# Performance work log

Hardware: AMD Instinct MI355X
Metric: run time of the kernel (lower is better)

The kernel has to match this reference:

```python
import jax, jax.numpy as jnp
import numpy as np
from jax import lax

B, C, IC, H, W = 4, 64, 32, 64, 64


def _conv(x, w, b, stride, pad):
    y = lax.conv_general_dilated(
        x, w, (stride, stride), [(pad, pad), (pad, pad)],
        dimension_numbers=('NCHW', 'OIHW', 'NCHW'))
    return y + b[None, :, None, None]


def setup_inputs() -> dict:
    key = jax.random.key(0)
    ks = jax.random.split(key, 15)
    s = 0.05
    inp = {
        'x': jax.random.normal(ks[0], (B, C, H, W), jnp.float32),
        # GEunit convs (3x3)
        'd1_w': jax.random.normal(ks[1], (C, C, 3, 3), jnp.float32) * s,
        'd1_b': jax.random.normal(ks[2], (C,), jnp.float32) * s,
        'd2_w': jax.random.normal(ks[3], (C, C, 3, 3), jnp.float32) * s,
        'd2_b': jax.random.normal(ks[4], (C,), jnp.float32) * s,
        'd3_w': jax.random.normal(ks[5], (C, C, 3, 3), jnp.float32) * s,
        'd3_b': jax.random.normal(ks[6], (C,), jnp.float32) * s,
        # 1x1 projections
        'g_w': jax.random.normal(ks[7], (IC, C, 1, 1), jnp.float32) * s,
        'g_b': jax.random.normal(ks[8], (IC,), jnp.float32) * s,
        'th_w': jax.random.normal(ks[9], (IC, C, 1, 1), jnp.float32) * s,
        'th_b': jax.random.normal(ks[10], (IC,), jnp.float32) * s,
        'ph_w': jax.random.normal(ks[11], (IC, C, 1, 1), jnp.float32) * s,
        'ph_b': jax.random.normal(ks[12], (IC,), jnp.float32) * s,
        # output projection (zero-init in original; random here for nontrivial baseline)
        'w_w': jax.random.normal(ks[13], (C, IC, 1, 1), jnp.float32) * s,
        'w_b': jax.random.normal(ks[14], (C,), jnp.float32) * s,
    }
    return inp


def _forward(x, d1_w, d1_b, d2_w, d2_b, d3_w, d3_b,
             g_w, g_b, th_w, th_b, ph_w, ph_b, w_w, w_b):
    lrelu = lambda v: jnp.where(v >= 0, v, 0.2 * v)
    y = lrelu(_conv(x, d1_w, d1_b, 2, 1))
    y = lrelu(_conv(y, d2_w, d2_b, 2, 1))
    y = _conv(y, d3_w, d3_b, 2, 1)
    y = jax.image.resize(y, (x.shape[0], x.shape[1], x.shape[2], x.shape[3]),
                         method='bilinear')  # align_corners=False equivalent
    am = jax.nn.sigmoid(y) * x  # attention_map, [B,C,H,W]

    b, c, h, w = am.shape
    n = h * w
    g_x = _conv(am, g_w, g_b, 1, 0).reshape(b, IC, n)      # [B,IC,N]
    theta = _conv(am, th_w, th_b, 1, 0).reshape(b, IC, n)  # [B,IC,N]
    phi = _conv(am, ph_w, ph_b, 1, 0).reshape(b, IC, n)    # [B,IC,N]

    # f[b,i,j] = theta[:, i] . phi[:, j];  softmax over dim=1 (the i axis)
    f = jnp.einsum('bci,bcj->bij', theta, phi)             # [B,N,N]
    f_div_C = jax.nn.softmax(f, axis=1)
    y2 = jnp.einsum('bij,bjc->bic', f_div_C, g_x.transpose(0, 2, 1))  # [B,N,IC]
    y2 = y2.transpose(0, 2, 1).reshape(b, IC, h, w)

    W_y = _conv(y2, w_w, w_b, 1, 0)
    z = W_y + am
    return z * x


def reference(x, d1_w, d1_b, d2_w, d2_b, d3_w, d3_b,
              g_w, g_b, th_w, th_b, ph_w, ph_b, w_w, w_b):
    return _forward(x, d1_w, d1_b, d2_w, d2_b, d3_w, d3_b,
                    g_w, g_b, th_w, th_b, ph_w, ph_b, w_w, w_b)
```

## Files before the change

kernel.cpp:

```cpp
#include <hip/hip_runtime.h>

#define B_ 4
#define C_ 64
#define IC_ 32
#define N_ 4096
#define LOG2E 1.44269504088896341f

typedef __attribute__((ext_vector_type(8))) short short8;
typedef __attribute__((ext_vector_type(4))) float floatx4;

__device__ __forceinline__ unsigned short f2bf(float f) {
  unsigned u = __float_as_uint(f);
  u += 0x7FFFu + ((u >> 16) & 1u);
  return (unsigned short)(u >> 16);
}
__device__ __forceinline__ float bf2f(unsigned short h) {
  return __uint_as_float(((unsigned)h) << 16);
}

__global__ void __launch_bounds__(256) pack_xw_k(
    const float* __restrict__ x, unsigned short* __restrict__ xclp,
    const float* __restrict__ d1_w, const float* __restrict__ d2_w, const float* __restrict__ d3_w,
    const float* __restrict__ th_w, const float* __restrict__ ph_w, const float* __restrict__ g_w,
    const float* __restrict__ th_b, const float* __restrict__ ph_b, const float* __restrict__ g_b,
    unsigned short* __restrict__ wpk, unsigned short* __restrict__ wproj, float* __restrict__ bproj,
    unsigned short* __restrict__ y1clp, unsigned short* __restrict__ y2clp)
{
  __shared__ float s[64][65];
  const int t = threadIdx.x;
  if (blockIdx.x < 256) {
    const int b = blockIdx.x >> 6, h = blockIdx.x & 63;
    for (int idx = t; idx < 4096; idx += 256) {
      int c = idx >> 6, w = idx & 63;
      s[c][w] = x[((size_t)(b * 64 + c)) * 4096 + h * 64 + w];
    }
    __syncthreads();
    for (int idx = t; idx < 4096; idx += 256) {
      int w = idx >> 6, c = idx & 63;
      xclp[(((size_t)b * 66 + h + 1) * 66 + (w + 1)) * 64 + c] = f2bf(s[c][w]);
    }
  } else {
    const int tid = (blockIdx.x - 256) * 256 + t;
    for (int idx = tid; idx < 3 * 36864; idx += 16 * 256) {
      int cv = idx / 36864, r = idx % 36864;
      int tap = r / 4096, r2 = r % 4096;
      int oc = r2 >> 6, ic = r2 & 63;
      const float* src = (cv == 0) ? d1_w : (cv == 1) ? d2_w : d3_w;
      wpk[(size_t)cv * 36864 + tap * 4096 + oc * 64 + ic] = f2bf(src[oc * 576 + ic * 9 + tap]);
    }
    for (int idx = tid; idx < 6144; idx += 16 * 256) {
      int m = idx >> 6, ic = idx & 63;
      float v = (m < 32) ? LOG2E * th_w[m * 64 + ic]
              : (m < 64) ? ph_w[(m - 32) * 64 + ic]
                         : g_w[(m - 64) * 64 + ic];
      wproj[m * 64 + ic] = f2bf(v);
    }
    for (int m = tid; m < 96; m += 16 * 256) {
      bproj[m] = (m < 32) ? LOG2E * th_b[m] : (m < 64) ? ph_b[m - 32] : g_b[m - 64];
    }
    const uint4 z4 = {0u, 0u, 0u, 0u};
    for (int idx = tid; idx < 4 * 4356; idx += 4096) {
      int r = idx % 4356, h = r / 66, w = r % 66;
      if (h == 0 || h == 65 || w == 0 || w == 65) {
        uint4* d = reinterpret_cast<uint4*>(xclp + (size_t)idx * 64);
#pragma unroll
        for (int q = 0; q < 8; ++q) d[q] = z4;
      }
    }
    for (int idx = tid; idx < 4 * 1156; idx += 4096) {
      int r = idx % 1156, h = r / 34, w = r % 34;
      if (h == 0 || h == 33 || w == 0 || w == 33) {
        uint4* d = reinterpret_cast<uint4*>(y1clp + (size_t)idx * 64);
#pragma unroll
        for (int q = 0; q < 8; ++q) d[q] = z4;
      }
    }
    for (int idx = tid; idx < 4 * 324; idx += 4096) {
      int r = idx % 324, h = r / 18, w = r % 18;
      if (h == 0 || h == 17 || w == 0 || w == 17) {
        uint4* d = reinterpret_cast<uint4*>(y2clp + (size_t)idx * 64);
#pragma unroll
        for (int q = 0; q < 8; ++q) d[q] = z4;
      }
    }
  }
}

template<int IN_PW, int OUT_H, bool LRELU, bool OUT_BF16>
__global__ void __launch_bounds__(64) convmf_k(
    const unsigned short* __restrict__ xin, const unsigned short* __restrict__ wp,
    const float* __restrict__ bias, unsigned short* __restrict__ obf,
    float* __restrict__ of32)
{
  constexpr int NTILES = OUT_H * OUT_H / 16;
  const int lane = threadIdx.x;
  const int n15 = lane & 15, quad = lane >> 4;
  int bx = blockIdx.x;
  const int octile = bx & 3; bx >>= 2;
  const int otile = bx % NTILES;
  const int b = bx / NTILES;
  const int o = otile * 16 + n15;
  const int oh = o / OUT_H, ow = o % OUT_H;
  const unsigned short* xb = xin + (size_t)b * IN_PW * IN_PW * 64;
  floatx4 acc = {0.f, 0.f, 0.f, 0.f};
#pragma unroll
  for (int tap = 0; tap < 9; ++tap) {
    const int kh = tap / 3, kw = tap % 3;
    const unsigned short* xpix = xb + ((size_t)(oh * 2 + kh) * IN_PW + (ow * 2 + kw)) * 64;
#pragma unroll
    for (int ks = 0; ks < 2; ++ks) {
      short8 af = *reinterpret_cast<const short8*>(
          wp + ((size_t)tap * 64 + octile * 16 + n15) * 64 + ks * 32 + quad * 8);
      short8 bf = *reinterpret_cast<const short8*>(xpix + ks * 32 + quad * 8);
      acc = __builtin_amdgcn_mfma_f32_16x16x32_bf16(af, bf, acc, 0, 0, 0);
    }
  }
  const float4 bv = *reinterpret_cast<const float4*>(bias + octile * 16 + quad * 4);
  float v[4] = {acc[0] + bv.x, acc[1] + bv.y, acc[2] + bv.z, acc[3] + bv.w};
  if (LRELU) {
#pragma unroll
    for (int r = 0; r < 4; ++r) v[r] = (v[r] >= 0.f) ? v[r] : 0.2f * v[r];
  }
  if (OUT_BF16) {
    constexpr int OPW = OUT_H + 2;
    unsigned short pk[4];
#pragma unroll
    for (int r = 0; r < 4; ++r) pk[r] = f2bf(v[r]);
    *reinterpret_cast<uint2*>(
        obf + (((size_t)b * OPW + oh + 1) * OPW + (ow + 1)) * 64 + octile * 16 + quad * 4) =
        *reinterpret_cast<uint2*>(pk);
  } else {
    *reinterpret_cast<float4*>(
        of32 + ((size_t)b * OUT_H * OUT_H + o) * 64 + octile * 16 + quad * 4) =
        *reinterpret_cast<float4*>(v);
  }
}

__global__ void __launch_bounds__(256) upsproj_k(
    const unsigned short* __restrict__ y2clp, const unsigned short* __restrict__ wp3,
    const float* __restrict__ b3, const float* __restrict__ x,
    const unsigned short* __restrict__ wproj, const float* __restrict__ bproj,
    unsigned short* __restrict__ am_cl, unsigned short* __restrict__ thph,
    unsigned short* __restrict__ g16)
{
  const int b = blockIdx.x >> 6, oh = blockIdx.x & 63;
  const int t = threadIdx.x;
  __shared__ float s0[512], s1[512];
  __shared__ unsigned short s_am[64][72];
  float sh = (oh + 0.5f) * 0.125f - 0.5f;
  float fh = floorf(sh); float ah = sh - fh; int h0 = (int)fh;
  int h0c = min(7, max(0, h0)), h1c = min(7, max(0, h0 + 1));
  {
    const int wave = t >> 6, lane = t & 63;
    const int n15 = lane & 15, quad = lane >> 4;
    const int hrow = (n15 < 8) ? h0c : h1c;
    const int ow8 = n15 & 7;
    const unsigned short* xb2 = y2clp + (size_t)b * 18 * 18 * 64;
    floatx4 acc = {0.f, 0.f, 0.f, 0.f};
#pragma unroll
    for (int tap = 0; tap < 9; ++tap) {
      const int kh = tap / 3, kw = tap % 3;
      const unsigned short* xpix = xb2 + ((size_t)(hrow * 2 + kh) * 18 + (ow8 * 2 + kw)) * 64;
#pragma unroll
      for (int ks = 0; ks < 2; ++ks) {
        short8 af = *reinterpret_cast<const short8*>(
            wp3 + ((size_t)tap * 64 + wave * 16 + n15) * 64 + ks * 32 + quad * 8);
        short8 bf = *reinterpret_cast<const short8*>(xpix + ks * 32 + quad * 8);
        acc = __builtin_amdgcn_mfma_f32_16x16x32_bf16(af, bf, acc, 0, 0, 0);
      }
    }
    const float4 bv = *reinterpret_cast<const float4*>(b3 + wave * 16 + quad * 4);
    float4 st = {acc[0] + bv.x, acc[1] + bv.y, acc[2] + bv.z, acc[3] + bv.w};
    float* dst = (n15 < 8) ? s0 : s1;
    *reinterpret_cast<float4*>(&dst[(size_t)ow8 * 64 + wave * 16 + quad * 4]) = st;
  }
  __syncthreads();
  {
    const int ow = t >> 2, cq = t & 3;
    float sw = (ow + 0.5f) * 0.125f - 0.5f;
    float fw = floorf(sw); float aw = sw - fw; int w0 = (int)fw;
    int w0c = min(7, max(0, w0)), w1c = min(7, max(0, w0 + 1));
    const int n = oh * 64 + ow;
    const float* xb = x + (size_t)b * 64 * 4096 + n;
    unsigned short* ap = am_cl + ((size_t)b * N_ + n) * 64 + cq * 16;
#pragma unroll
    for (int u = 0; u < 4; ++u) {
      int c0 = cq * 16 + u * 4;
      float4 a00 = *reinterpret_cast<const float4*>(&s0[w0c * 64 + c0]);
      float4 a01 = *reinterpret_cast<const float4*>(&s0[w1c * 64 + c0]);
      float4 a10 = *reinterpret_cast<const float4*>(&s1[w0c * 64 + c0]);
      float4 a11 = *reinterpret_cast<const float4*>(&s1[w1c * 64 + c0]);
      float i0[4] = {a00.x * (1.f - aw) + a01.x * aw, a00.y * (1.f - aw) + a01.y * aw,
                     a00.z * (1.f - aw) + a01.z * aw, a00.w * (1.f - aw) + a01.w * aw};
      float i1[4] = {a10.x * (1.f - aw) + a11.x * aw, a10.y * (1.f - aw) + a11.y * aw,
                     a10.z * (1.f - aw) + a11.z * aw, a10.w * (1.f - aw) + a11.w * aw};
      unsigned short pk[4];
#pragma unroll
      for (int vi = 0; vi < 4; ++vi) {
        float vv = i0[vi] * (1.f - ah) + i1[vi] * ah;
        float xv = xb[(size_t)(c0 + vi) * 4096];
        float sig = 1.f / (1.f + __expf(-vv));
        pk[vi] = f2bf(sig * xv);
      }
      uint2 pkt = *reinterpret_cast<uint2*>(pk);
      *reinterpret_cast<uint2*>(ap + u * 4) = pkt;
      *reinterpret_cast<uint2*>(&s_am[ow][c0]) = pkt;
    }
  }
  __syncthreads();
  const int wave = t >> 6, lane = t & 63;
  const int n15 = lane & 15, quad = lane >> 4;
  const int n = oh * 64 + wave * 16 + n15;
  const unsigned short* srow = &s_am[wave * 16 + n15][0];
  const short8 bf0 = *reinterpret_cast<const short8*>(srow + quad * 8);
  const short8 bf1 = *reinterpret_cast<const short8*>(srow + 32 + quad * 8);
#pragma unroll
  for (int mt = 0; mt < 6; ++mt) {
    short8 a0 = *reinterpret_cast<const short8*>(wproj + ((size_t)mt * 16 + n15) * 64 + quad * 8);
    short8 a1 = *reinterpret_cast<const short8*>(wproj + ((size_t)mt * 16 + n15) * 64 + 32 + quad * 8);
    floatx4 acc = {0.f, 0.f, 0.f, 0.f};
    acc = __builtin_amdgcn_mfma_f32_16x16x32_bf16(a0, bf0, acc, 0, 0, 0);
    acc = __builtin_amdgcn_mfma_f32_16x16x32_bf16(a1, bf1, acc, 0, 0, 0);
    const float4 bv = *reinterpret_cast<const float4*>(bproj + mt * 16 + quad * 4);
    float v[4] = {acc[0] + bv.x, acc[1] + bv.y, acc[2] + bv.z, acc[3] + bv.w};
    if (mt < 4) {
      unsigned short pk[4];
#pragma unroll
      for (int r = 0; r < 4; ++r) pk[r] = f2bf(v[r]);
      *reinterpret_cast<uint2*>(thph + ((size_t)b * N_ + n) * 64 + mt * 16 + quad * 4) =
          *reinterpret_cast<uint2*>(pk);
    } else {
#pragma unroll
      for (int r = 0; r < 4; ++r)
        g16[((size_t)b * 32 + (mt - 4) * 16 + quad * 4 + r) * N_ + n] = f2bf(v[r]);
    }
  }
}

__global__ void __launch_bounds__(256) attn_stats_k(
    const unsigned short* __restrict__ thph, float* __restrict__ lpart)
{
  const int b  = blockIdx.y;
  const int iz = blockIdx.z;
  const int t = threadIdx.x, wave = t >> 6, lane = t & 63;
  const int n15 = lane & 15, quad = lane >> 4;
  const int jw = blockIdx.x * 512 + wave * 128;
  const unsigned short* base = thph + (size_t)b * N_ * 64;
  short8 bv[8];
#pragma unroll
  for (int v = 0; v < 8; ++v)
    bv[v] = *reinterpret_cast<const short8*>(base + (size_t)(jw + v * 16 + n15) * 64 + 32 + quad * 8);
  float ls[8];
#pragma unroll
  for (int v = 0; v < 8; ++v) ls[v] = 0.f;
  const unsigned short* ap = base + (size_t)(iz * 256 + n15) * 64 + quad * 8;
  short8 ac = *reinterpret_cast<const short8*>(ap);
  for (int st = 0; st < 16; ++st) {
    short8 an = *reinterpret_cast<const short8*>(ap + (size_t)((st < 15) ? st + 1 : st) * 1024);
#pragma unroll
    for (int v = 0; v < 8; ++v) {
      floatx4 z = {0.f, 0.f, 0.f, 0.f};
      z = __builtin_amdgcn_mfma_f32_16x16x32_bf16(ac, bv[v], z, 0, 0, 0);
      ls[v] += (__builtin_amdgcn_exp2f(z[0]) + __builtin_amdgcn_exp2f(z[1]))
             + (__builtin_amdgcn_exp2f(z[2]) + __builtin_amdgcn_exp2f(z[3]));
    }
    ac = an;
  }
#pragma unroll
  for (int v = 0; v < 8; ++v) {
    ls[v] += __shfl_xor(ls[v], 16);
    ls[v] += __shfl_xor(ls[v], 32);
  }
  if (quad == 0) {
#pragma unroll
    for (int v = 0; v < 8; ++v)
      lpart[((size_t)iz * B_ + b) * N_ + jw + v * 16 + n15] = ls[v];
  }
}

#define PHI_PITCH 40
#define G_PITCH   136
__global__ void __launch_bounds__(256, 2) attn_pv_k(
    const unsigned short* __restrict__ thph, const unsigned short* __restrict__ g16,
    const float* __restrict__ lpart, unsigned short* __restrict__ y2p)
{
  const int b  = blockIdx.y;
  const int jq = blockIdx.z;
  const int t = threadIdx.x, wave = t >> 6, lane = t & 63;
  const int n15 = lane & 15, quad = lane >> 4;
  const int iw = blockIdx.x * 128 + wave * 32;
  const unsigned short* base = thph + (size_t)b * N_ * 64;
  const unsigned short* gs   = g16  + (size_t)b * 32 * N_;
  __shared__ unsigned short phi_lds[2][128 * PHI_PITCH];
  __shared__ unsigned short g_lds[2][32 * G_PITCH];
  __shared__ float rl_lds[1024];

  const int jbase = jq * 1024;
  for (int jj = t; jj < 1024; jj += 256) {
    float l = 0.f;
#pragma unroll
    for (int iz = 0; iz < 16; ++iz) l += lpart[((size_t)iz * B_ + b) * N_ + jbase + jj];
    rl_lds[jj] = 1.f / l;
  }

  const short8 bth0 = *reinterpret_cast<const short8*>(base + (size_t)(iw + n15) * 64 + quad * 8);
  const short8 bth1 = *reinterpret_cast<const short8*>(base + (size_t)(iw + 16 + n15) * 64 + quad * 8);
  floatx4 Y00 = {0.f, 0.f, 0.f, 0.f}, Y01 = {0.f, 0.f, 0.f, 0.f};
  floatx4 Y10 = {0.f, 0.f, 0.f, 0.f}, Y11 = {0.f, 0.f, 0.f, 0.f};

  const int rphi = wave * 32 + (lane >> 2), cph = lane & 3;
  const int cg   = wave * 8  + (lane >> 4), chg = lane & 15;

  uint4 sp0, sp1, sg0, sg1;
  sp0 = *reinterpret_cast<const uint4*>(base + (size_t)(jbase + rphi) * 64 + 32 + cph * 8);
  sp1 = *reinterpret_cast<const uint4*>(base + (size_t)(jbase + rphi + 16) * 64 + 32 + cph * 8);
  sg0 = *reinterpret_cast<const uint4*>(gs + (size_t)cg * N_ + jbase + chg * 8);
  sg1 = *reinterpret_cast<const uint4*>(gs + (size_t)(cg + 4) * N_ + jbase + chg * 8);
  __syncthreads();

#define PV_WRITE_STAGE(BUF, CHN)                                                     \
  {                                                                                  \
    *reinterpret_cast<uint4*>(&phi_lds[BUF][rphi * PHI_PITCH + cph * 8]) = sp0;      \
    *reinterpret_cast<uint4*>(&phi_lds[BUF][(rphi + 16) * PHI_PITCH + cph * 8]) = sp1;\
    const int jloc = (CHN) * 128 + chg * 8;                                          \
    float4 r0 = *reinterpret_cast<const float4*>(&rl_lds[jloc]);                     \
    float4 r1 = *reinterpret_cast<const float4*>(&rl_lds[jloc + 4]);                 \
    union U8s { uint4 u4; unsigned short us[8]; } ua, ub, oa, ob_;                   \
    ua.u4 = sg0; ub.u4 = sg1;                                                        \
    oa.us[0] = f2bf(bf2f(ua.us[0]) * r0.x); oa.us[1] = f2bf(bf2f(ua.us[1]) * r0.y);  \
    oa.us[2] = f2bf(bf2f(ua.us[2]) * r0.z); oa.us[3] = f2bf(bf2f(ua.us[3]) * r0.w);  \
    oa.us[4] = f2bf(bf2f(ua.us[4]) * r1.x); oa.us[5] = f2bf(bf2f(ua.us[5]) * r1.y);  \
    oa.us[6] = f2bf(bf2f(ua.us[6]) * r1.z); oa.us[7] = f2bf(bf2f(ua.us[7]) * r1.w);  \
    ob_.us[0] = f2bf(bf2f(ub.us[0]) * r0.x); ob_.us[1] = f2bf(bf2f(ub.us[1]) * r0.y);\
    ob_.us[2] = f2bf(bf2f(ub.us[2]) * r0.z); ob_.us[3] = f2bf(bf2f(ub.us[3]) * r0.w);\
    ob_.us[4] = f2bf(bf2f(ub.us[4]) * r1.x); ob_.us[5] = f2bf(bf2f(ub.us[5]) * r1.y);\
    ob_.us[6] = f2bf(bf2f(ub.us[6]) * r1.z); ob_.us[7] = f2bf(bf2f(ub.us[7]) * r1.w);\
    *reinterpret_cast<uint4*>(&g_lds[BUF][cg * G_PITCH + chg * 8]) = oa.u4;          \
    *reinterpret_cast<uint4*>(&g_lds[BUF][(cg + 4) * G_PITCH + chg * 8]) = ob_.u4;   \
  }

  PV_WRITE_STAGE(0, 0)
  __syncthreads();

  int j0 = jbase;
  for (int ch = 0; ch < 8; ++ch, j0 += 128) {
    const int cur = ch & 1;
    if (ch < 7) {
      const int jn = j0 + 128;
      sp0 = *reinterpret_cast<const uint4*>(base + (size_t)(jn + rphi) * 64 + 32 + cph * 8);
      sp1 = *reinterpret_cast<const uint4*>(base + (size_t)(jn + rphi + 16) * 64 + 32 + cph * 8);
      sg0 = *reinterpret_cast<const uint4*>(gs + (size_t)cg * N_ + jn + chg * 8);
      sg1 = *reinterpret_cast<const uint4*>(gs + (size_t)(cg + 4) * N_ + jn + chg * 8);
    }
    const unsigned short* phb = &phi_lds[cur][0];
    const unsigned short* glb = &g_lds[cur][0];
#pragma unroll
    for (int sg = 0; sg < 4; ++sg) {
      unsigned pk0[4], pk1[4];
#pragma unroll
      for (int jtl = 0; jtl < 2; ++jtl) {
        const int jt = sg * 2 + jtl;
        short8 aph = *reinterpret_cast<const short8*>(phb + (jt * 16 + n15) * PHI_PITCH + quad * 8);
        floatx4 z0 = {0.f, 0.f, 0.f, 0.f}, z1 = {0.f, 0.f, 0.f, 0.f};
        z0 = __builtin_amdgcn_mfma_f32_16x16x32_bf16(aph, bth0, z0, 0, 0, 0);
        z1 = __builtin_amdgcn_mfma_f32_16x16x32_bf16(aph, bth1, z1, 0, 0, 0);
        float a0 = __builtin_amdgcn_exp2f(z0[0]), a1 = __builtin_amdgcn_exp2f(z0[1]);
        float a2 = __builtin_amdgcn_exp2f(z0[2]), a3 = __builtin_amdgcn_exp2f(z0[3]);
        float b0f = __builtin_amdgcn_exp2f(z1[0]), b1f = __builtin_amdgcn_exp2f(z1[1]);
        float b2f = __builtin_amdgcn_exp2f(z1[2]), b3f = __builtin_amdgcn_exp2f(z1[3]);
        pk0[jtl * 2 + 0] = __builtin_amdgcn_perm(__float_as_uint(a1), __float_as_uint(a0), 0x07060302);
        pk0[jtl * 2 + 1] = __builtin_amdgcn_perm(__float_as_uint(a3), __float_as_uint(a2), 0x07060302);
        pk1[jtl * 2 + 0] = __builtin_amdgcn_perm(__float_as_uint(b1f), __float_as_uint(b0f), 0x07060302);
        pk1[jtl * 2 + 1] = __builtin_amdgcn_perm(__float_as_uint(b3f), __float_as_uint(b2f), 0x07060302);
      }
      union { unsigned u[4]; short8 v; } pa0, pa1, gb0, gb1;
      pa0.u[0] = pk0[0]; pa0.u[1] = pk0[1]; pa0.u[2] = pk0[2]; pa0.u[3] = pk0[3];
      pa1.u[0] = pk1[0]; pa1.u[1] = pk1[1]; pa1.u[2] = pk1[2]; pa1.u[3] = pk1[3];
      const unsigned short* gr0 = glb + n15 * G_PITCH + sg * 32 + quad * 4;
      const unsigned short* gr1 = glb + (16 + n15) * G_PITCH + sg * 32 + quad * 4;
      uint2 lo0 = *reinterpret_cast<const uint2*>(gr0);
      uint2 hi0 = *reinterpret_cast<const uint2*>(gr0 + 16);
      uint2 lo1 = *reinterpret_cast<const uint2*>(gr1);
      uint2 hi1 = *reinterpret_cast<const uint2*>(gr1 + 16);
      gb0.u[0] = lo0.x; gb0.u[1] = lo0.y; gb0.u[2] = hi0.x; gb0.u[3] = hi0.y;
      gb1.u[0] = lo1.x; gb1.u[1] = lo1.y; gb1.u[2] = hi1.x; gb1.u[3] = hi1.y;
      Y00 = __builtin_amdgcn_mfma_f32_16x16x32_bf16(pa0.v, gb0.v, Y00, 0, 0, 0);
      Y01 = __builtin_amdgcn_mfma_f32_16x16x32_bf16(pa0.v, gb1.v, Y01, 0, 0, 0);
      Y10 = __builtin_amdgcn_mfma_f32_16x16x32_bf16(pa1.v, gb0.v, Y10, 0, 0, 0);
      Y11 = __builtin_amdgcn_mfma_f32_16x16x32_bf16(pa1.v, gb1.v, Y11, 0, 0, 0);
    }
    if (ch < 7) {
      const int nb = cur ^ 1;
      PV_WRITE_STAGE(nb, ch + 1)
    }
    __syncthreads();
  }
#undef PV_WRITE_STAGE
  unsigned w00[2], w01[2], w10[2], w11[2];
  w00[0] = ((unsigned)f2bf(Y00[1]) << 16) | f2bf(Y00[0]);
  w00[1] = ((unsigned)f2bf(Y00[3]) << 16) | f2bf(Y00[2]);
  w01[0] = ((unsigned)f2bf(Y01[1]) << 16) | f2bf(Y01[0]);
  w01[1] = ((unsigned)f2bf(Y01[3]) << 16) | f2bf(Y01[2]);
  w10[0] = ((unsigned)f2bf(Y10[1]) << 16) | f2bf(Y10[0]);
  w10[1] = ((unsigned)f2bf(Y10[3]) << 16) | f2bf(Y10[2]);
  w11[0] = ((unsigned)f2bf(Y11[1]) << 16) | f2bf(Y11[0]);
  w11[1] = ((unsigned)f2bf(Y11[3]) << 16) | f2bf(Y11[2]);
  const size_t orow = ((size_t)jq * B_ + b) * 32;
  *reinterpret_cast<uint2*>(y2p + (orow + n15) * N_ + iw + quad * 4) =
      *reinterpret_cast<uint2*>(w00);
  *reinterpret_cast<uint2*>(y2p + (orow + 16 + n15) * N_ + iw + quad * 4) =
      *reinterpret_cast<uint2*>(w01);
  *reinterpret_cast<uint2*>(y2p + (orow + n15) * N_ + iw + 16 + quad * 4) =
      *reinterpret_cast<uint2*>(w10);
  *reinterpret_cast<uint2*>(y2p + (orow + 16 + n15) * N_ + iw + 16 + quad * 4) =
      *reinterpret_cast<uint2*>(w11);
}

__global__ void __launch_bounds__(256) final_k(
    const unsigned short* __restrict__ y2p, const float* __restrict__ w_w,
    const float* __restrict__ w_b, const unsigned short* __restrict__ am_cl,
    const float* __restrict__ x, float* __restrict__ out)
{
  const int n0 = (blockIdx.x * 256 + threadIdx.x) * 2;
  const int o0 = blockIdx.y * 8;
  const int b  = blockIdx.z;
  float a0[8], a1[8];
#pragma unroll
  for (int u = 0; u < 8; ++u) { a0[u] = w_b[o0 + u]; a1[u] = a0[u]; }
  for (int c = 0; c < 32; ++c) {
    float s0 = 0.f, s1 = 0.f;
#pragma unroll
    for (int ph = 0; ph < 4; ++ph) {
      unsigned v = *reinterpret_cast<const unsigned*>(
          y2p + (((size_t)ph * B_ + b) * 32 + c) * N_ + n0);
      s0 += bf2f((unsigned short)(v & 0xffffu));
      s1 += bf2f((unsigned short)(v >> 16));
    }
#pragma unroll
    for (int u = 0; u < 8; ++u) {
      float wv = w_w[(o0 + u) * 32 + c];
      a0[u] += wv * s0; a1[u] += wv * s1;
    }
  }
  const short8 am0 = *reinterpret_cast<const short8*>(am_cl + ((size_t)b * N_ + n0) * 64 + o0);
  const short8 am1 = *reinterpret_cast<const short8*>(am_cl + ((size_t)b * N_ + n0 + 1) * 64 + o0);
#pragma unroll
  for (int u = 0; u < 8; ++u) {
    size_t off = ((size_t)b * 64 + o0 + u) * N_ + n0;
    float2 xv = *reinterpret_cast<const float2*>(x + off);
    float2 ov;
    ov.x = (a0[u] + bf2f((unsigned short)am0[u])) * xv.x;
    ov.y = (a1[u] + bf2f((unsigned short)am1[u])) * xv.y;
    *reinterpret_cast<float2*>(out + off) = ov;
  }
}

extern "C" void kernel_launch(void* const* d_in, const int* in_sizes, int n_in,
                              void* d_out, int out_size, void* d_ws, size_t ws_size,
                              hipStream_t stream) {
  const float* x    = (const float*)d_in[0];
  const float* d1_w = (const float*)d_in[1];
  const float* d1_b = (const float*)d_in[2];
  const float* d2_w = (const float*)d_in[3];
  const float* d2_b = (const float*)d_in[4];
  const float* d3_w = (const float*)d_in[5];
  const float* d3_b = (const float*)d_in[6];
  const float* g_w  = (const float*)d_in[7];
  const float* g_b  = (const float*)d_in[8];
  const float* th_w = (const float*)d_in[9];
  const float* th_b = (const float*)d_in[10];
  const float* ph_w = (const float*)d_in[11];
  const float* ph_b = (const float*)d_in[12];
  const float* w_w  = (const float*)d_in[13];
  const float* w_b  = (const float*)d_in[14];
  float* out = (float*)d_out;

  char* p = (char*)d_ws;
  unsigned short* am_cl = (unsigned short*)p;  p += (size_t)B_ * N_ * 64 * 2;
  unsigned short* thph  = (unsigned short*)p;  p += (size_t)B_ * N_ * 64 * 2;
  unsigned short* g16   = (unsigned short*)p;  p += (size_t)B_ * 32 * N_ * 2;
  float* lpart          = (float*)p;           p += (size_t)16 * B_ * N_ * 4;
  unsigned short* y2p   = (unsigned short*)p;  p += (size_t)4 * B_ * 32 * N_ * 2;
  unsigned short* wpk   = (unsigned short*)p;  p += (size_t)3 * 36864 * 2;
  unsigned short* wproj = (unsigned short*)p;  p += (size_t)96 * 64 * 2;
  float* bproj          = (float*)p;           p += (size_t)96 * 4;
  unsigned short* xclp  = (unsigned short*)p;  p += (size_t)B_ * 66 * 66 * 64 * 2;
  unsigned short* y1clp = (unsigned short*)p;  p += (size_t)B_ * 34 * 34 * 64 * 2;
  unsigned short* y2clp = (unsigned short*)p;  p += (size_t)B_ * 18 * 18 * 64 * 2;

  pack_xw_k<<<272, 256, 0, stream>>>(x, xclp, d1_w, d2_w, d3_w, th_w, ph_w, g_w,
                                     th_b, ph_b, g_b, wpk, wproj, bproj, y1clp, y2clp);
  convmf_k<66, 32, true,  true ><<<1024, 64, 0, stream>>>(xclp,  wpk,         d1_b, y1clp, nullptr);
  convmf_k<34, 16, true,  true ><<<256,  64, 0, stream>>>(y1clp, wpk + 36864, d2_b, y2clp, nullptr);
  upsproj_k<<<256, 256, 0, stream>>>(y2clp, wpk + 2 * 36864, d3_b, x, wproj, bproj,
                                     am_cl, thph, g16);
  attn_stats_k<<<dim3(8, 4, 16), 256, 0, stream>>>(thph, lpart);
  attn_pv_k<<<dim3(32, 4, 4), 256, 0, stream>>>(thph, g16, lpart, y2p);
  final_k<<<dim3(8, 8, 4), 256, 0, stream>>>(y2p, w_w, w_b, am_cl, x, out);
}
```

Measured before the change: 152.5 us.

## Retile conv, attention PV and final kernels; pad upsample LDS rows

The stride-2 conv kernel now computes two 16-channel output tiles per wave, reusing each input fragment across two MFMAs and halving the grid. The attention PV kernel gives each wave 64 query rows instead of 32 and splits the key axis into 8 partitions of 512 instead of 4 of 1024, so it issues more MFMAs per loaded phi/g tile and writes twice as many partial outputs. The final kernel first reduces the 8 partials into shared memory and then has each thread compute 16 output channels. The upsample LDS rows are padded from 64 to 68 floats to avoid bank conflicts. In exchange there are more registers per wave in the PV kernel and more partial-sum traffic.

```diff
diff --git a/kernel.cpp b/kernel.cpp
--- a/kernel.cpp
+++ b/kernel.cpp
@@ -86,54 +86,52 @@
   }
 }
 
-template<int IN_PW, int OUT_H, bool LRELU, bool OUT_BF16>
+template<int IN_PW, int OUT_H>
 __global__ void __launch_bounds__(64) convmf_k(
     const unsigned short* __restrict__ xin, const unsigned short* __restrict__ wp,
-    const float* __restrict__ bias, unsigned short* __restrict__ obf,
-    float* __restrict__ of32)
+    const float* __restrict__ bias, unsigned short* __restrict__ obf)
 {
   constexpr int NTILES = OUT_H * OUT_H / 16;
   const int lane = threadIdx.x;
   const int n15 = lane & 15, quad = lane >> 4;
   int bx = blockIdx.x;
-  const int octile = bx & 3; bx >>= 2;
+  const int opair = bx & 1; bx >>= 1;
   const int otile = bx % NTILES;
   const int b = bx / NTILES;
   const int o = otile * 16 + n15;
   const int oh = o / OUT_H, ow = o % OUT_H;
   const unsigned short* xb = xin + (size_t)b * IN_PW * IN_PW * 64;
-  floatx4 acc = {0.f, 0.f, 0.f, 0.f};
+  floatx4 acc0 = {0.f, 0.f, 0.f, 0.f}, acc1 = {0.f, 0.f, 0.f, 0.f};
 #pragma unroll
   for (int tap = 0; tap < 9; ++tap) {
     const int kh = tap / 3, kw = tap % 3;
     const unsigned short* xpix = xb + ((size_t)(oh * 2 + kh) * IN_PW + (ow * 2 + kw)) * 64;
 #pragma unroll
     for (int ks = 0; ks < 2; ++ks) {
-      short8 af = *reinterpret_cast<const short8*>(
-          wp + ((size_t)tap * 64 + octile * 16 + n15) * 64 + ks * 32 + quad * 8);
       short8 bf = *reinterpret_cast<const short8*>(xpix + ks * 32 + quad * 8);
-      acc = __builtin_amdgcn_mfma_f32_16x16x32_bf16(af, bf, acc, 0, 0, 0);
-    }
-  }
-  const float4 bv = *reinterpret_cast<const float4*>(bias + octile * 16 + quad * 4);
-  float v[4] = {acc[0] + bv.x, acc[1] + bv.y, acc[2] + bv.z, acc[3] + bv.w};
-  if (LRELU) {
-#pragma unroll
-    for (int r = 0; r < 4; ++r) v[r] = (v[r] >= 0.f) ? v[r] : 0.2f * v[r];
-  }
-  if (OUT_BF16) {
-    constexpr int OPW = OUT_H + 2;
-    unsigned short pk[4];
-#pragma unroll
-    for (int r = 0; r < 4; ++r) pk[r] = f2bf(v[r]);
-    *reinterpret_cast<uint2*>(
-        obf + (((size_t)b * OPW + oh + 1) * OPW + (ow + 1)) * 64 + octile * 16 + quad * 4) =
-        *reinterpret_cast<uint2*>(pk);
-  } else {
-    *reinterpret_cast<float4*>(
-        of32 + ((size_t)b * OUT_H * OUT_H + o) * 64 + octile * 16 + quad * 4) =
-        *reinterpret_cast<float4*>(v);
-  }
+      short8 af0 = *reinterpret_cast<const short8*>(
+          wp + ((size_t)tap * 64 + (opair * 2 + 0) * 16 + n15) * 64 + ks * 32 + quad * 8);
+      short8 af1 = *reinterpret_cast<const short8*>(
+          wp + ((size_t)tap * 64 + (opair * 2 + 1) * 16 + n15) * 64 + ks * 32 + quad * 8);
+      acc0 = __builtin_amdgcn_mfma_f32_16x16x32_bf16(af0, bf, acc0, 0, 0, 0);
+      acc1 = __builtin_amdgcn_mfma_f32_16x16x32_bf16(af1, bf, acc1, 0, 0, 0);
+    }
+  }
+  constexpr int OPW = OUT_H + 2;
+  const float4 bv0 = *reinterpret_cast<const float4*>(bias + (opair * 2 + 0) * 16 + quad * 4);
+  const float4 bv1 = *reinterpret_cast<const float4*>(bias + (opair * 2 + 1) * 16 + quad * 4);
+  float v0[4] = {acc0[0] + bv0.x, acc0[1] + bv0.y, acc0[2] + bv0.z, acc0[3] + bv0.w};
+  float v1[4] = {acc1[0] + bv1.x, acc1[1] + bv1.y, acc1[2] + bv1.z, acc1[3] + bv1.w};
+  unsigned short pk0[4], pk1[4];
+#pragma unroll
+  for (int r = 0; r < 4; ++r) {
+    v0[r] = (v0[r] >= 0.f) ? v0[r] : 0.2f * v0[r];
+    v1[r] = (v1[r] >= 0.f) ? v1[r] : 0.2f * v1[r];
+    pk0[r] = f2bf(v0[r]); pk1[r] = f2bf(v1[r]);
+  }
+  unsigned short* orow = obf + (((size_t)b * OPW + oh + 1) * OPW + (ow + 1)) * 64;
+  *reinterpret_cast<uint2*>(orow + (opair * 2 + 0) * 16 + quad * 4) = *reinterpret_cast<uint2*>(pk0);
+  *reinterpret_cast<uint2*>(orow + (opair * 2 + 1) * 16 + quad * 4) = *reinterpret_cast<uint2*>(pk1);
 }
 
 __global__ void __launch_bounds__(256) upsproj_k(
@@ -145,7 +143,7 @@
 {
   const int b = blockIdx.x >> 6, oh = blockIdx.x & 63;
   const int t = threadIdx.x;
-  __shared__ float s0[512], s1[512];
+  __shared__ float s0[8 * 68], s1[8 * 68];
   __shared__ unsigned short s_am[64][72];
   float sh = (oh + 0.5f) * 0.125f - 0.5f;
   float fh = floorf(sh); float ah = sh - fh; int h0 = (int)fh;
@@ -172,7 +170,7 @@
     const float4 bv = *reinterpret_cast<const float4*>(b3 + wave * 16 + quad * 4);
     float4 st = {acc[0] + bv.x, acc[1] + bv.y, acc[2] + bv.z, acc[3] + bv.w};
     float* dst = (n15 < 8) ? s0 : s1;
-    *reinterpret_cast<float4*>(&dst[(size_t)ow8 * 64 + wave * 16 + quad * 4]) = st;
+    *reinterpret_cast<float4*>(&dst[(size_t)ow8 * 68 + wave * 16 + quad * 4]) = st;
   }
   __syncthreads();
   {
@@ -186,10 +184,10 @@
 #pragma unroll
     for (int u = 0; u < 4; ++u) {
       int c0 = cq * 16 + u * 4;
-      float4 a00 = *reinterpret_cast<const float4*>(&s0[w0c * 64 + c0]);
-      float4 a01 = *reinterpret_cast<const float4*>(&s0[w1c * 64 + c0]);
-      float4 a10 = *reinterpret_cast<const float4*>(&s1[w0c * 64 + c0]);
-      float4 a11 = *reinterpret_cast<const float4*>(&s1[w1c * 64 + c0]);
+      float4 a00 = *reinterpret_cast<const float4*>(&s0[w0c * 68 + c0]);
+      float4 a01 = *reinterpret_cast<const float4*>(&s0[w1c * 68 + c0]);
+      float4 a10 = *reinterpret_cast<const float4*>(&s1[w0c * 68 + c0]);
+      float4 a11 = *reinterpret_cast<const float4*>(&s1[w1c * 68 + c0]);
       float i0[4] = {a00.x * (1.f - aw) + a01.x * aw, a00.y * (1.f - aw) + a01.y * aw,
                      a00.z * (1.f - aw) + a01.z * aw, a00.w * (1.f - aw) + a01.w * aw};
       float i1[4] = {a10.x * (1.f - aw) + a11.x * aw, a10.y * (1.f - aw) + a11.y * aw,
@@ -285,28 +283,34 @@
     const float* __restrict__ lpart, unsigned short* __restrict__ y2p)
 {
   const int b  = blockIdx.y;
-  const int jq = blockIdx.z;
+  const int jh = blockIdx.z;
   const int t = threadIdx.x, wave = t >> 6, lane = t & 63;
   const int n15 = lane & 15, quad = lane >> 4;
-  const int iw = blockIdx.x * 128 + wave * 32;
+  const int iw0 = blockIdx.x * 256 + wave * 64;
   const unsigned short* base = thph + (size_t)b * N_ * 64;
   const unsigned short* gs   = g16  + (size_t)b * 32 * N_;
   __shared__ unsigned short phi_lds[2][128 * PHI_PITCH];
   __shared__ unsigned short g_lds[2][32 * G_PITCH];
-  __shared__ float rl_lds[1024];
-
-  const int jbase = jq * 1024;
-  for (int jj = t; jj < 1024; jj += 256) {
+  __shared__ float rl_lds[512];
+
+  const int jbase = jh * 512;
+  for (int jj = t; jj < 512; jj += 256) {
     float l = 0.f;
 #pragma unroll
     for (int iz = 0; iz < 16; ++iz) l += lpart[((size_t)iz * B_ + b) * N_ + jbase + jj];
     rl_lds[jj] = 1.f / l;
   }
 
-  const short8 bth0 = *reinterpret_cast<const short8*>(base + (size_t)(iw + n15) * 64 + quad * 8);
-  const short8 bth1 = *reinterpret_cast<const short8*>(base + (size_t)(iw + 16 + n15) * 64 + quad * 8);
-  floatx4 Y00 = {0.f, 0.f, 0.f, 0.f}, Y01 = {0.f, 0.f, 0.f, 0.f};
-  floatx4 Y10 = {0.f, 0.f, 0.f, 0.f}, Y11 = {0.f, 0.f, 0.f, 0.f};
+  short8 bth[4];
+#pragma unroll
+  for (int k = 0; k < 4; ++k)
+    bth[k] = *reinterpret_cast<const short8*>(base + (size_t)(iw0 + k * 16 + n15) * 64 + quad * 8);
+  floatx4 Y[4][2];
+#pragma unroll
+  for (int k = 0; k < 4; ++k) {
+    Y[k][0] = floatx4{0.f, 0.f, 0.f, 0.f};
+    Y[k][1] = floatx4{0.f, 0.f, 0.f, 0.f};
+  }
 
   const int rphi = wave * 32 + (lane >> 2), cph = lane & 3;
   const int cg   = wave * 8  + (lane >> 4), chg = lane & 15;
@@ -343,9 +347,9 @@
   __syncthreads();
 
   int j0 = jbase;
-  for (int ch = 0; ch < 8; ++ch, j0 += 128) {
+  for (int ch = 0; ch < 4; ++ch, j0 += 128) {
     const int cur = ch & 1;
-    if (ch < 7) {
+    if (ch < 3) {
       const int jn = j0 + 128;
       sp0 = *reinterpret_cast<const uint4*>(base + (size_t)(jn + rphi) * 64 + 32 + cph * 8);
       sp1 = *reinterpret_cast<const uint4*>(base + (size_t)(jn + rphi + 16) * 64 + 32 + cph * 8);
@@ -356,26 +360,26 @@
     const unsigned short* glb = &g_lds[cur][0];
 #pragma unroll
     for (int sg = 0; sg < 4; ++sg) {
-      unsigned pk0[4], pk1[4];
+      unsigned pk[4][4];
 #pragma unroll
       for (int jtl = 0; jtl < 2; ++jtl) {
         const int jt = sg * 2 + jtl;
         short8 aph = *reinterpret_cast<const short8*>(phb + (jt * 16 + n15) * PHI_PITCH + quad * 8);
-        floatx4 z0 = {0.f, 0.f, 0.f, 0.f}, z1 = {0.f, 0.f, 0.f, 0.f};
-        z0 = __builtin_amdgcn_mfma_f32_16x16x32_bf16(aph, bth0, z0, 0, 0, 0);
-        z1 = __builtin_amdgcn_mfma_f32_16x16x32_bf16(aph, bth1, z1, 0, 0, 0);
-        float a0 = __builtin_amdgcn_exp2f(z0[0]), a1 = __builtin_amdgcn_exp2f(z0[1]);
-        float a2 = __builtin_amdgcn_exp2f(z0[2]), a3 = __builtin_amdgcn_exp2f(z0[3]);
-        float b0f = __builtin_amdgcn_exp2f(z1[0]), b1f = __builtin_amdgcn_exp2f(z1[1]);
-        float b2f = __builtin_amdgcn_exp2f(z1[2]), b3f = __builtin_amdgcn_exp2f(z1[3]);
-        pk0[jtl * 2 + 0] = __builtin_amdgcn_perm(__float_as_uint(a1), __float_as_uint(a0), 0x07060302);
-        pk0[jtl * 2 + 1] = __builtin_amdgcn_perm(__float_as_uint(a3), __float_as_uint(a2), 0x07060302);
-        pk1[jtl * 2 + 0] = __builtin_amdgcn_perm(__float_as_uint(b1f), __float_as_uint(b0f), 0x07060302);
-        pk1[jtl * 2 + 1] = __builtin_amdgcn_perm(__float_as_uint(b3f), __float_as_uint(b2f), 0x07060302);
-      }
-      union { unsigned u[4]; short8 v; } pa0, pa1, gb0, gb1;
-      pa0.u[0] = pk0[0]; pa0.u[1] = pk0[1]; pa0.u[2] = pk0[2]; pa0.u[3] = pk0[3];
-      pa1.u[0] = pk1[0]; pa1.u[1] = pk1[1]; pa1.u[2] = pk1[2]; pa1.u[3] = pk1[3];
+        floatx4 z[4];
+#pragma unroll
+        for (int k = 0; k < 4; ++k) {
+          floatx4 zz = {0.f, 0.f, 0.f, 0.f};
+          z[k] = __builtin_amdgcn_mfma_f32_16x16x32_bf16(aph, bth[k], zz, 0, 0, 0);
+        }
+#pragma unroll
+        for (int k = 0; k < 4; ++k) {
+          float e0 = __builtin_amdgcn_exp2f(z[k][0]), e1 = __builtin_amdgcn_exp2f(z[k][1]);
+          float e2 = __builtin_amdgcn_exp2f(z[k][2]), e3 = __builtin_amdgcn_exp2f(z[k][3]);
+          pk[k][jtl * 2 + 0] = __builtin_amdgcn_perm(__float_as_uint(e1), __float_as_uint(e0), 0x07060302);
+          pk[k][jtl * 2 + 1] = __builtin_amdgcn_perm(__float_as_uint(e3), __float_as_uint(e2), 0x07060302);
+        }
+      }
+      union { unsigned u[4]; short8 v; } gb0, gb1;
       const unsigned short* gr0 = glb + n15 * G_PITCH + sg * 32 + quad * 4;
       const unsigned short* gr1 = glb + (16 + n15) * G_PITCH + sg * 32 + quad * 4;
       uint2 lo0 = *reinterpret_cast<const uint2*>(gr0);
@@ -384,36 +388,34 @@
       uint2 hi1 = *reinterpret_cast<const uint2*>(gr1 + 16);
       gb0.u[0] = lo0.x; gb0.u[1] = lo0.y; gb0.u[2] = hi0.x; gb0.u[3] = hi0.y;
       gb1.u[0] = lo1.x; gb1.u[1] = lo1.y; gb1.u[2] = hi1.x; gb1.u[3] = hi1.y;
-      Y00 = __builtin_amdgcn_mfma_f32_16x16x32_bf16(pa0.v, gb0.v, Y00, 0, 0, 0);
-      Y01 = __builtin_amdgcn_mfma_f32_16x16x32_bf16(pa0.v, gb1.v, Y01, 0, 0, 0);
-      Y10 = __builtin_amdgcn_mfma_f32_16x16x32_bf16(pa1.v, gb0.v, Y10, 0, 0, 0);
-      Y11 = __builtin_amdgcn_mfma_f32_16x16x32_bf16(pa1.v, gb1.v, Y11, 0, 0, 0);
-    }
-    if (ch < 7) {
+#pragma unroll
+      for (int k = 0; k < 4; ++k) {
+        union { unsigned u[4]; short8 v; } pa;
+        pa.u[0] = pk[k][0]; pa.u[1] = pk[k][1]; pa.u[2] = pk[k][2]; pa.u[3] = pk[k][3];
+        Y[k][0] = __builtin_amdgcn_mfma_f32_16x16x32_bf16(pa.v, gb0.v, Y[k][0], 0, 0, 0);
+        Y[k][1] = __builtin_amdgcn_mfma_f32_16x16x32_bf16(pa.v, gb1.v, Y[k][1], 0, 0, 0);
+      }
+    }
+    if (ch < 3) {
       const int nb = cur ^ 1;
       PV_WRITE_STAGE(nb, ch + 1)
     }
     __syncthreads();
   }
 #undef PV_WRITE_STAGE
-  unsigned w00[2], w01[2], w10[2], w11[2];
-  w00[0] = ((unsigned)f2bf(Y00[1]) << 16) | f2bf(Y00[0]);
-  w00[1] = ((unsigned)f2bf(Y00[3]) << 16) | f2bf(Y00[2]);
-  w01[0] = ((unsigned)f2bf(Y01[1]) << 16) | f2bf(Y01[0]);
-  w01[1] = ((unsigned)f2bf(Y01[3]) << 16) | f2bf(Y01[2]);
-  w10[0] = ((unsigned)f2bf(Y10[1]) << 16) | f2bf(Y10[0]);
-  w10[1] = ((unsigned)f2bf(Y10[3]) << 16) | f2bf(Y10[2]);
-  w11[0] = ((unsigned)f2bf(Y11[1]) << 16) | f2bf(Y11[0]);
-  w11[1] = ((unsigned)f2bf(Y11[3]) << 16) | f2bf(Y11[2]);
-  const size_t orow = ((size_t)jq * B_ + b) * 32;
-  *reinterpret_cast<uint2*>(y2p + (orow + n15) * N_ + iw + quad * 4) =
-      *reinterpret_cast<uint2*>(w00);
-  *reinterpret_cast<uint2*>(y2p + (orow + 16 + n15) * N_ + iw + quad * 4) =
-      *reinterpret_cast<uint2*>(w01);
-  *reinterpret_cast<uint2*>(y2p + (orow + n15) * N_ + iw + 16 + quad * 4) =
-      *reinterpret_cast<uint2*>(w10);
-  *reinterpret_cast<uint2*>(y2p + (orow + 16 + n15) * N_ + iw + 16 + quad * 4) =
-      *reinterpret_cast<uint2*>(w11);
+  const size_t orow = ((size_t)jh * B_ + b) * 32;
+#pragma unroll
+  for (int k = 0; k < 4; ++k) {
+    unsigned w0[2], w1[2];
+    w0[0] = ((unsigned)f2bf(Y[k][0][1]) << 16) | f2bf(Y[k][0][0]);
+    w0[1] = ((unsigned)f2bf(Y[k][0][3]) << 16) | f2bf(Y[k][0][2]);
+    w1[0] = ((unsigned)f2bf(Y[k][1][1]) << 16) | f2bf(Y[k][1][0]);
+    w1[1] = ((unsigned)f2bf(Y[k][1][3]) << 16) | f2bf(Y[k][1][2]);
+    *reinterpret_cast<uint2*>(y2p + (orow + n15) * N_ + iw0 + k * 16 + quad * 4) =
+        *reinterpret_cast<uint2*>(w0);
+    *reinterpret_cast<uint2*>(y2p + (orow + 16 + n15) * N_ + iw0 + k * 16 + quad * 4) =
+        *reinterpret_cast<uint2*>(w1);
+  }
 }
 
 __global__ void __launch_bounds__(256) final_k(
@@ -421,37 +423,40 @@
     const float* __restrict__ w_b, const unsigned short* __restrict__ am_cl,
     const float* __restrict__ x, float* __restrict__ out)
 {
-  const int n0 = (blockIdx.x * 256 + threadIdx.x) * 2;
-  const int o0 = blockIdx.y * 8;
+  __shared__ float sred[32 * 128];
+  const int t = threadIdx.x;
+  const int xw = blockIdx.x;
+  const int yh = blockIdx.y;
   const int b  = blockIdx.z;
-  float a0[8], a1[8];
-#pragma unroll
-  for (int u = 0; u < 8; ++u) { a0[u] = w_b[o0 + u]; a1[u] = a0[u]; }
+  for (int idx = t; idx < 4096; idx += 256) {
+    const int c = idx >> 7, nl = idx & 127;
+    const int n = xw * 128 + nl;
+    float sv = 0.f;
+#pragma unroll
+    for (int ph = 0; ph < 8; ++ph)
+      sv += bf2f(y2p[(((size_t)ph * B_ + b) * 32 + c) * N_ + n]);
+    sred[idx] = sv;
+  }
+  __syncthreads();
+  const int nl = t & 127, sub = t >> 7;
+  const int n = xw * 128 + nl;
+  const int o0 = yh * 32 + sub * 16;
+  float a[16];
+#pragma unroll
+  for (int u = 0; u < 16; ++u) a[u] = w_b[o0 + u];
   for (int c = 0; c < 32; ++c) {
-    float s0 = 0.f, s1 = 0.f;
-#pragma unroll
-    for (int ph = 0; ph < 4; ++ph) {
-      unsigned v = *reinterpret_cast<const unsigned*>(
-          y2p + (((size_t)ph * B_ + b) * 32 + c) * N_ + n0);
-      s0 += bf2f((unsigned short)(v & 0xffffu));
-      s1 += bf2f((unsigned short)(v >> 16));
-    }
-#pragma unroll
-    for (int u = 0; u < 8; ++u) {
-      float wv = w_w[(o0 + u) * 32 + c];
-      a0[u] += wv * s0; a1[u] += wv * s1;
-    }
-  }
-  const short8 am0 = *reinterpret_cast<const short8*>(am_cl + ((size_t)b * N_ + n0) * 64 + o0);
-  const short8 am1 = *reinterpret_cast<const short8*>(am_cl + ((size_t)b * N_ + n0 + 1) * 64 + o0);
-#pragma unroll
-  for (int u = 0; u < 8; ++u) {
-    size_t off = ((size_t)b * 64 + o0 + u) * N_ + n0;
-    float2 xv = *reinterpret_cast<const float2*>(x + off);
-    float2 ov;
-    ov.x = (a0[u] + bf2f((unsigned short)am0[u])) * xv.x;
-    ov.y = (a1[u] + bf2f((unsigned short)am1[u])) * xv.y;
-    *reinterpret_cast<float2*>(out + off) = ov;
+    const float sv = sred[c * 128 + nl];
+#pragma unroll
+    for (int u = 0; u < 16; ++u) a[u] += w_w[(o0 + u) * 32 + c] * sv;
+  }
+  const unsigned short* amp = am_cl + ((size_t)b * N_ + n) * 64 + o0;
+  const short8 am0 = *reinterpret_cast<const short8*>(amp);
+  const short8 am1 = *reinterpret_cast<const short8*>(amp + 8);
+#pragma unroll
+  for (int u = 0; u < 16; ++u) {
+    const size_t off = ((size_t)b * 64 + o0 + u) * N_ + n;
+    const float amv = bf2f((unsigned short)((u < 8) ? am0[u] : am1[u - 8]));
+    out[off] = (a[u] + amv) * x[off];
   }
 }
 
@@ -480,7 +485,7 @@
   unsigned short* thph  = (unsigned short*)p;  p += (size_t)B_ * N_ * 64 * 2;
   unsigned short* g16   = (unsigned short*)p;  p += (size_t)B_ * 32 * N_ * 2;
   float* lpart          = (float*)p;           p += (size_t)16 * B_ * N_ * 4;
-  unsigned short* y2p   = (unsigned short*)p;  p += (size_t)4 * B_ * 32 * N_ * 2;
+  unsigned short* y2p   = (unsigned short*)p;  p += (size_t)8 * B_ * 32 * N_ * 2;
   unsigned short* wpk   = (unsigned short*)p;  p += (size_t)3 * 36864 * 2;
   unsigned short* wproj = (unsigned short*)p;  p += (size_t)96 * 64 * 2;
   float* bproj          = (float*)p;           p += (size_t)96 * 4;
@@ -490,11 +495,11 @@
 
   pack_xw_k<<<272, 256, 0, stream>>>(x, xclp, d1_w, d2_w, d3_w, th_w, ph_w, g_w,
                                      th_b, ph_b, g_b, wpk, wproj, bproj, y1clp, y2clp);
-  convmf_k<66, 32, true,  true ><<<1024, 64, 0, stream>>>(xclp,  wpk,         d1_b, y1clp, nullptr);
-  convmf_k<34, 16, true,  true ><<<256,  64, 0, stream>>>(y1clp, wpk + 36864, d2_b, y2clp, nullptr);
+  convmf_k<66, 32><<<512, 64, 0, stream>>>(xclp,  wpk,         d1_b, y1clp);
+  convmf_k<34, 16><<<128, 64, 0, stream>>>(y1clp, wpk + 36864, d2_b, y2clp);
   upsproj_k<<<256, 256, 0, stream>>>(y2clp, wpk + 2 * 36864, d3_b, x, wproj, bproj,
                                      am_cl, thph, g16);
   attn_stats_k<<<dim3(8, 4, 16), 256, 0, stream>>>(thph, lpart);
-  attn_pv_k<<<dim3(32, 4, 4), 256, 0, stream>>>(thph, g16, lpart, y2p);
-  final_k<<<dim3(8, 8, 4), 256, 0, stream>>>(y2p, w_w, w_b, am_cl, x, out);
-}
+  attn_pv_k<<<dim3(16, 4, 8), 256, 0, stream>>>(thph, g16, lpart, y2p);
+  final_k<<<dim3(32, 2, 4), 256, 0, stream>>>(y2p, w_w, w_b, am_cl, x, out);
+}
```

New measurement: 154.6 us. Within noise of the previous version (+1.4%).
